# Optimization experiments

Measured on AMD Instinct MI355X. Metric: run time of the kernel, lower is better.

## Reference

```python
import jax, jax.numpy as jnp
import numpy as np

N = 50000      # num nodes
E = 600000     # num edges
D = 128        # num_node_features (in == out)
R = 8          # num_relations


def setup_inputs() -> dict:
    key = jax.random.key(0)
    k = jax.random.split(key, 6)
    x = jax.random.normal(k[0], (N, D), dtype=jnp.float32)
    edge_index = jax.random.randint(k[1], (2, E), 0, N, dtype=jnp.int32)
    edge_type = jax.random.randint(k[2], (E,), 0, R, dtype=jnp.int32)
    scale = 1.0 / np.sqrt(D).astype(np.float32)
    weight = jax.random.normal(k[3], (R, D, D), dtype=jnp.float32) * scale  # per-relation W_r
    root = jax.random.normal(k[4], (D, D), dtype=jnp.float32) * scale       # self-loop weight
    bias = jnp.zeros((D,), dtype=jnp.float32)
    return {"x": x, "edge_index": edge_index, "edge_type": edge_type,
            "weight": weight, "root": root, "bias": bias}


def _rgcn(x, weight, root, bias, edge_index, edge_type):
    # RGCNConv (PyG defaults: aggr='mean' per relation, root weight + bias)
    src, dst = edge_index[0], edge_index[1]
    # combined segment id over (relation, dst) so one segment_sum covers all relations
    seg = edge_type * N + dst                              # [E]
    msgs = x[src]                                          # [E, D] gather
    sums = jax.ops.segment_sum(msgs, seg, num_segments=R * N)                 # [R*N, D]
    cnts = jax.ops.segment_sum(jnp.ones((E, 1), x.dtype), seg, num_segments=R * N)
    mean = sums / jnp.maximum(cnts, 1.0)                   # mean over neighbors, 0 if none
    agg = mean.reshape(R, N, D)
    out = jnp.einsum('rnd,rde->ne', agg, weight) + x @ root + bias
    return out


def reference(x, edge_index, edge_type, weight, root, bias):
    return jax.nn.relu(_rgcn(x, weight, root, bias, edge_index, edge_type))
```

## Files before the change

### kernel.cpp

```cpp
#include <hip/hip_runtime.h>

constexpr int NN = 50000;
constexpr int NE = 600000;
constexpr int D  = 128;
constexpr int NR = 8;
constexpr int KT = (NR + 1) * D;
constexpr int NSEG = NN * NR;

constexpr int SCAN_ELEMS = 1024;
constexpr int NBLK2 = (NSEG + SCAN_ELEMS - 1) / SCAN_ELEMS;

constexpr int BM = 128;
constexpr int GEMM_GRID = (NN + BM - 1) / BM;

typedef unsigned int   u32;
typedef unsigned short u16;
typedef float  f32x4 __attribute__((ext_vector_type(4)));
typedef short  s16x8 __attribute__((ext_vector_type(8)));

__device__ __forceinline__ u16 f2bf(float f) {
    u32 u = __float_as_uint(f);
    u32 r = (u + 0x7fffu + ((u >> 16) & 1u)) >> 16;
    return (u16)r;
}

__device__ __forceinline__ void async_cp16(const void* g, void* l) {
    __builtin_amdgcn_global_load_lds(
        (const __attribute__((address_space(1))) u32*)g,
        (__attribute__((address_space(3))) u32*)l, 16, 0, 0);
}

__global__ __launch_bounds__(256) void prep_all(const float* __restrict__ x,
                                                const float* __restrict__ weight,
                                                const float* __restrict__ root,
                                                const int* __restrict__ dst,
                                                const int* __restrict__ et,
                                                u16* __restrict__ xb,
                                                u16* __restrict__ wt9,
                                                int* __restrict__ cnt2) {
    const int NX4 = NN * D / 4;
    const int NW  = (NR + 1) * D * D;
    int gid = blockIdx.x * 256 + threadIdx.x;
    if (gid < NX4) {
        int i = gid * 4;
        float4 v = *(const float4*)(x + i);
        ushort4 o;
        o.x = f2bf(v.x); o.y = f2bf(v.y); o.z = f2bf(v.z); o.w = f2bf(v.w);
        *(ushort4*)(xb + i) = o;
        return;
    }
    int g = gid - NX4;
    if (g < NW) {
        int p = g >> 14;
        int idx = g & 16383;
        int n = idx >> 7, k = idx & 127;
        float v = (p == 0) ? root[k * D + n]
                           : weight[(size_t)(p - 1) * D * D + k * D + n];
        wt9[(size_t)p * 16384 + idx] = f2bf(v);
        return;
    }
    int e = g - NW;
    if (e < NE) atomicAdd(&cnt2[dst[e] * NR + et[e]], 1);
}

__global__ __launch_bounds__(256) void scan1(const int* __restrict__ cnt,
                                             int* __restrict__ offs,
                                             int* __restrict__ bsums) {
    __shared__ int lds[256];
    int t = threadIdx.x;
    int base = blockIdx.x * SCAN_ELEMS + t * 4;
    int v0 = (base + 0 < NSEG) ? cnt[base + 0] : 0;
    int v1 = (base + 1 < NSEG) ? cnt[base + 1] : 0;
    int v2 = (base + 2 < NSEG) ? cnt[base + 2] : 0;
    int v3 = (base + 3 < NSEG) ? cnt[base + 3] : 0;
    int s = v0 + v1 + v2 + v3;
    lds[t] = s;
    __syncthreads();
    int val = s;
    for (int off = 1; off < 256; off <<= 1) {
        int tmp = (t >= off) ? lds[t - off] : 0;
        __syncthreads();
        val += tmp;
        lds[t] = val;
        __syncthreads();
    }
    int ex = val - s;
    if (base + 0 < NSEG) offs[base + 0] = ex;
    if (base + 1 < NSEG) offs[base + 1] = ex + v0;
    if (base + 2 < NSEG) offs[base + 2] = ex + v0 + v1;
    if (base + 3 < NSEG) offs[base + 3] = ex + v0 + v1 + v2;
    if (t == 255) bsums[blockIdx.x] = val;
}

__global__ __launch_bounds__(512) void scan2(int* __restrict__ bsums) {
    __shared__ int lds[512];
    int t = threadIdx.x;
    int v = (t < NBLK2) ? bsums[t] : 0;
    lds[t] = v;
    __syncthreads();
    int val = v;
    for (int off = 1; off < 512; off <<= 1) {
        int tmp = (t >= off) ? lds[t - off] : 0;
        __syncthreads();
        val += tmp;
        lds[t] = val;
        __syncthreads();
    }
    if (t < NBLK2) bsums[t] = val - v;
}

__global__ __launch_bounds__(256) void scan3(int* __restrict__ offs,
                                             int* __restrict__ cur,
                                             const int* __restrict__ bsums) {
    int i = blockIdx.x * 256 + threadIdx.x;
    if (i < NSEG) {
        int v = offs[i] + bsums[i >> 10];
        offs[i] = v;
        cur[i]  = v;
    }
    if (i == 0) offs[NSEG] = NE;
}

__global__ __launch_bounds__(256) void fill_bins(const int* __restrict__ src,
                                                 const int* __restrict__ dst,
                                                 const int* __restrict__ et,
                                                 int* __restrict__ cur,
                                                 int* __restrict__ ebin) {
    int e = blockIdx.x * 256 + threadIdx.x;
    if (e >= NE) return;
    int r = et[e];
    int idx = atomicAdd(&cur[dst[e] * NR + r], 1);
    ebin[idx] = (r << 16) | src[e];
}

__global__ __launch_bounds__(128) void aggregate_kernel(const u32* __restrict__ xw,
                                                        const int* __restrict__ offs2,
                                                        const int* __restrict__ ebin,
                                                        u32* __restrict__ sw) {
    const int lane = threadIdx.x & 63;
    const int n = blockIdx.x * 2 + (threadIdx.x >> 6);
    if (n >= NN) return;
    const int beg = __builtin_amdgcn_readfirstlane(offs2[n * NR]);
    const int c   = __builtin_amdgcn_readfirstlane(offs2[n * NR + NR]) - beg;

    float a0 = 0.f, a1 = 0.f;
    int r_cur = 0, cnt_cur = 0;

    int q0 = 0, q1 = 0, q2 = 0, q3 = 0, q4 = 0, q5 = 0, q6 = 0, q7 = 0;
    u32 v0 = 0, v1 = 0, v2 = 0, v3 = 0, v4 = 0, v5 = 0, v6 = 0, v7 = 0;

#define REFILL(Q, V, IDX)                                                   \
    if ((IDX) < c) {                                                        \
        Q = __builtin_amdgcn_readfirstlane(ebin[beg + (IDX)]);              \
        V = xw[(size_t)((u32)Q & 0xffffu) * 64 + lane];                     \
    }
#define FLUSH()                                                             \
    {                                                                       \
        float inv_ = 1.0f / (float)(cnt_cur > 0 ? cnt_cur : 1);             \
        u32 lo16_ = f2bf(a0 * inv_);                                        \
        u32 hi16_ = f2bf(a1 * inv_);                                        \
        sw[((size_t)r_cur * NN + n) * 64 + lane] = lo16_ | (hi16_ << 16);   \
        a0 = 0.f; a1 = 0.f; cnt_cur = 0; ++r_cur;                           \
    }
#define CONSUME(Q, V)                                                       \
    {                                                                       \
        int rj_ = (int)((u32)(Q) >> 16);                                    \
        while (r_cur < rj_) FLUSH()                                         \
        a0 += __uint_as_float((V) << 16);                                   \
        a1 += __uint_as_float((V) & 0xffff0000u);                           \
        ++cnt_cur;                                                          \
    }

    REFILL(q0, v0, 0) REFILL(q1, v1, 1) REFILL(q2, v2, 2) REFILL(q3, v3, 3)
    REFILL(q4, v4, 4) REFILL(q5, v5, 5) REFILL(q6, v6, 6) REFILL(q7, v7, 7)

    int e = 0;
    for (; e + 8 <= c; e += 8) {
        CONSUME(q0, v0) REFILL(q0, v0, e + 8)
        CONSUME(q1, v1) REFILL(q1, v1, e + 9)
        CONSUME(q2, v2) REFILL(q2, v2, e + 10)
        CONSUME(q3, v3) REFILL(q3, v3, e + 11)
        CONSUME(q4, v4) REFILL(q4, v4, e + 12)
        CONSUME(q5, v5) REFILL(q5, v5, e + 13)
        CONSUME(q6, v6) REFILL(q6, v6, e + 14)
        CONSUME(q7, v7) REFILL(q7, v7, e + 15)
    }
    if (e + 0 < c) CONSUME(q0, v0)
    if (e + 1 < c) CONSUME(q1, v1)
    if (e + 2 < c) CONSUME(q2, v2)
    if (e + 3 < c) CONSUME(q3, v3)
    if (e + 4 < c) CONSUME(q4, v4)
    if (e + 5 < c) CONSUME(q5, v5)
    if (e + 6 < c) CONSUME(q6, v6)
    if (e + 7 < c) CONSUME(q7, v7)

    while (r_cur < NR) FLUSH()
#undef REFILL
#undef FLUSH
#undef CONSUME
}

__global__ __launch_bounds__(256) void mfma_gemm(const u16* __restrict__ xb,
                                                 const u16* __restrict__ sums,
                                                 const u16* __restrict__ wt9,
                                                 const float* __restrict__ bias,
                                                 float* __restrict__ out) {
    __shared__ __align__(16) u16 Bs[2][128 * 64];

    const int tid  = threadIdx.x;
    const int wave = tid >> 6;
    const int lane = tid & 63;
    const int m0   = blockIdx.x * BM;
    const int fr   = lane & 15;
    const int l4   = lane >> 4;
    const int fk   = l4 * 8;

    int boff[4];
#pragma unroll
    for (int r = 0; r < 4; ++r) {
        int p = r * 256 + tid;
        int g = p ^ ((p >> 3) & 7);
        boff[r] = (g >> 3) * D + (g & 7) * 8;
    }
    int bidx[16];
#pragma unroll
    for (int h = 0; h < 2; ++h)
#pragma unroll
        for (int nt = 0; nt < 8; ++nt) {
            int gl = (nt * 16 + fr) * 8 + h * 4 + l4;
            int pp = gl ^ ((gl >> 3) & 7);
            bidx[h * 8 + nt] = pp * 8;
        }

    int r0 = m0 + wave * 32 + fr;       if (r0 > NN - 1) r0 = NN - 1;
    int r1 = m0 + wave * 32 + 16 + fr;  if (r1 > NN - 1) r1 = NN - 1;
    const size_t aoff0 = (size_t)r0 * D + fk;
    const size_t aoff1 = (size_t)r1 * D + fk;

    auto stage = [&](u16* bufp, const u16* Bp) {
#pragma unroll
        for (int r = 0; r < 4; ++r)
            async_cp16(Bp + boff[r], (char*)bufp + (size_t)(r * 256 + tid) * 16);
    };

    f32x4 acc0[8], acc1[8];
#pragma unroll
    for (int j = 0; j < 8; ++j) {
        acc0[j] = (f32x4){0.f, 0.f, 0.f, 0.f};
        acc1[j] = (f32x4){0.f, 0.f, 0.f, 0.f};
    }

    s16x8 a0c, a1c, a2c, a3c, a0n1, a1n1, a2n1, a3n1, a0n2, a1n2, a2n2, a3n2;

    stage(&Bs[0][0], wt9);
    a0c  = *(const s16x8*)(xb + aoff0);
    a1c  = *(const s16x8*)(xb + aoff0 + 32);
    a2c  = *(const s16x8*)(xb + aoff1);
    a3c  = *(const s16x8*)(xb + aoff1 + 32);
    a0n1 = *(const s16x8*)(xb + aoff0 + 64);
    a1n1 = *(const s16x8*)(xb + aoff0 + 96);
    a2n1 = *(const s16x8*)(xb + aoff1 + 64);
    a3n1 = *(const s16x8*)(xb + aoff1 + 96);
    a0n2 = a0n1; a1n2 = a1n1; a2n2 = a2n1; a3n2 = a3n1;
    __builtin_amdgcn_sched_barrier(0);

    for (int it = 0; it < 17; ++it) {
        const int nx  = it + 1;
        const int npl = nx >> 1;
        const int kof = (nx & 1) * 64;
        u16* nbuf = &Bs[nx & 1][0];
        const u16* cbuf = &Bs[it & 1][0];

        stage(nbuf, wt9 + npl * 16384 + kof);
        if (it + 2 <= 17) {
            const int p2 = (it + 2) >> 1;
            const int k2 = ((it + 2) & 1) * 64;
            const u16* Ap2 = ((p2 == 0) ? xb
                              : sums + (size_t)(p2 - 1) * NN * D) + k2;
            a0n2 = *(const s16x8*)(Ap2 + aoff0);
            a1n2 = *(const s16x8*)(Ap2 + aoff0 + 32);
            a2n2 = *(const s16x8*)(Ap2 + aoff1);
            a3n2 = *(const s16x8*)(Ap2 + aoff1 + 32);
        }
        __builtin_amdgcn_sched_barrier(0);
        if (it < 16) { asm volatile("s_waitcnt vmcnt(12)" ::: "memory"); }
        else         { asm volatile("s_waitcnt vmcnt(8)"  ::: "memory"); }
        __builtin_amdgcn_s_barrier();
        __builtin_amdgcn_sched_barrier(0);
#pragma unroll
        for (int nt = 0; nt < 8; ++nt) {
            s16x8 bf = *(const s16x8*)(cbuf + bidx[nt]);
            acc0[nt] = __builtin_amdgcn_mfma_f32_16x16x32_bf16(a0c, bf, acc0[nt], 0, 0, 0);
            acc1[nt] = __builtin_amdgcn_mfma_f32_16x16x32_bf16(a2c, bf, acc1[nt], 0, 0, 0);
        }
#pragma unroll
        for (int nt = 0; nt < 8; ++nt) {
            s16x8 bf = *(const s16x8*)(cbuf + bidx[8 + nt]);
            acc0[nt] = __builtin_amdgcn_mfma_f32_16x16x32_bf16(a1c, bf, acc0[nt], 0, 0, 0);
            acc1[nt] = __builtin_amdgcn_mfma_f32_16x16x32_bf16(a3c, bf, acc1[nt], 0, 0, 0);
        }
        asm volatile("s_waitcnt lgkmcnt(0)" ::: "memory");
        __builtin_amdgcn_sched_barrier(0);
        __builtin_amdgcn_s_barrier();
        __builtin_amdgcn_sched_barrier(0);
        a0c = a0n1; a1c = a1n1; a2c = a2n1; a3c = a3n1;
        a0n1 = a0n2; a1n1 = a1n2; a2n1 = a2n2; a3n1 = a3n2;
    }
    asm volatile("s_waitcnt vmcnt(0)" ::: "memory");
    __builtin_amdgcn_s_barrier();
    __builtin_amdgcn_sched_barrier(0);
    {
        const u16* cbuf = &Bs[1][0];
#pragma unroll
        for (int nt = 0; nt < 8; ++nt) {
            s16x8 bf = *(const s16x8*)(cbuf + bidx[nt]);
            acc0[nt] = __builtin_amdgcn_mfma_f32_16x16x32_bf16(a0c, bf, acc0[nt], 0, 0, 0);
            acc1[nt] = __builtin_amdgcn_mfma_f32_16x16x32_bf16(a2c, bf, acc1[nt], 0, 0, 0);
        }
#pragma unroll
        for (int nt = 0; nt < 8; ++nt) {
            s16x8 bf = *(const s16x8*)(cbuf + bidx[8 + nt]);
            acc0[nt] = __builtin_amdgcn_mfma_f32_16x16x32_bf16(a1c, bf, acc0[nt], 0, 0, 0);
            acc1[nt] = __builtin_amdgcn_mfma_f32_16x16x32_bf16(a3c, bf, acc1[nt], 0, 0, 0);
        }
    }

    const int cl = lane & 15;
    const int rq = l4 * 4;
#pragma unroll
    for (int nt = 0; nt < 8; ++nt) {
        int col = nt * 16 + cl;
        float bv = bias[col];
#pragma unroll
        for (int reg = 0; reg < 4; ++reg) {
            int n = m0 + wave * 32 + rq + reg;
            if (n < NN) {
                float v = acc0[nt][reg] + bv;
                out[(size_t)n * D + col] = fmaxf(v, 0.0f);
            }
            int n2 = n + 16;
            if (n2 < NN) {
                float v = acc1[nt][reg] + bv;
                out[(size_t)n2 * D + col] = fmaxf(v, 0.0f);
            }
        }
    }
}

extern "C" void kernel_launch(void* const* d_in, const int* in_sizes, int n_in,
                              void* d_out, int out_size, void* d_ws, size_t ws_size,
                              hipStream_t stream) {
    const float* x      = (const float*)d_in[0];
    const int*   ei     = (const int*)d_in[1];
    const int*   et     = (const int*)d_in[2];
    const float* weight = (const float*)d_in[3];
    const float* root   = (const float*)d_in[4];
    const float* bias   = (const float*)d_in[5];
    float* out = (float*)d_out;
    const int* srcv = ei;
    const int* dstv = ei + NE;

    int* cnt2  = (int*)d_ws;
    int* cur2  = cnt2 + NSEG;
    int* offs2 = cur2 + NSEG;
    int* bsums = offs2 + NSEG + 1;
    int* ebin  = bsums + 512;
    size_t fixed_b  = ((char*)(ebin + NE) - (char*)d_ws);
    size_t fixed_al = (fixed_b + 255) & ~(size_t)255;
    u16* xb   = (u16*)((char*)d_ws + fixed_al);
    u16* sums = xb + (size_t)NN * D;
    u16* wt9  = sums + (size_t)NR * NN * D;

    hipMemsetAsync(cnt2, 0, NSEG * sizeof(int), stream);

    const int PREP = NN * D / 4 + (NR + 1) * D * D + NE;
    prep_all<<<(PREP + 255) / 256, 256, 0, stream>>>(x, weight, root, dstv, et,
                                                     xb, wt9, cnt2);

    scan1<<<NBLK2, 256, 0, stream>>>(cnt2, offs2, bsums);
    scan2<<<1, 512, 0, stream>>>(bsums);
    scan3<<<(NSEG + 256) / 256, 256, 0, stream>>>(offs2, cur2, bsums);
    fill_bins<<<(NE + 255) / 256, 256, 0, stream>>>(srcv, dstv, et, cur2, ebin);

    aggregate_kernel<<<(NN + 1) / 2, 128, 0, stream>>>((const u32*)xb, offs2, ebin,
                                                       (u32*)sums);

    mfma_gemm<<<GEMM_GRID, 256, 0, stream>>>(xb, sums, wt9, bias, out);
}
```

Before: 215.8 us.

## Skip storing empty relation segments; GEMM reads a zero page instead

The aggregation kernel no longer writes mean rows for (node, relation) segments that have no edges. The GEMM derives a per-row empty-relation bitmask from the CSR offsets and points the A-fragment loads for those rows at a small zeroed workspace page instead of the sums buffer. This removes both the write and the later read of empty bf16 rows, which are a sizeable share at the average degree here. In exchange each GEMM row does extra offset loads and address selects, and correctness now depends on the zero page staying zeroed.

New measurement: 216.1 us. No clear change (+0.1%).

```diff
diff --git a/kernel.cpp b/kernel.cpp
--- a/kernel.cpp
+++ b/kernel.cpp
@@ -4,7 +4,6 @@
 constexpr int NE = 600000;
 constexpr int D  = 128;
 constexpr int NR = 8;
-constexpr int KT = (NR + 1) * D;
 constexpr int NSEG = NN * NR;
 
 constexpr int SCAN_ELEMS = 1024;
@@ -156,11 +155,14 @@
     }
 #define FLUSH()                                                             \
     {                                                                       \
-        float inv_ = 1.0f / (float)(cnt_cur > 0 ? cnt_cur : 1);             \
-        u32 lo16_ = f2bf(a0 * inv_);                                        \
-        u32 hi16_ = f2bf(a1 * inv_);                                        \
-        sw[((size_t)r_cur * NN + n) * 64 + lane] = lo16_ | (hi16_ << 16);   \
-        a0 = 0.f; a1 = 0.f; cnt_cur = 0; ++r_cur;                           \
+        if (cnt_cur > 0) {                                                  \
+            float inv_ = 1.0f / (float)cnt_cur;                             \
+            u32 lo16_ = f2bf(a0 * inv_);                                    \
+            u32 hi16_ = f2bf(a1 * inv_);                                    \
+            sw[((size_t)r_cur * NN + n) * 64 + lane] = lo16_ | (hi16_ << 16);\
+            a0 = 0.f; a1 = 0.f; cnt_cur = 0;                                \
+        }                                                                   \
+        ++r_cur;                                                            \
     }
 #define CONSUME(Q, V)                                                       \
     {                                                                       \
@@ -204,6 +206,8 @@
                                                  const u16* __restrict__ sums,
                                                  const u16* __restrict__ wt9,
                                                  const float* __restrict__ bias,
+                                                 const int* __restrict__ offs2,
+                                                 const u16* __restrict__ zp,
                                                  float* __restrict__ out) {
     __shared__ __align__(16) u16 Bs[2][128 * 64];
 
@@ -236,6 +240,27 @@
     int r1 = m0 + wave * 32 + 16 + fr;  if (r1 > NN - 1) r1 = NN - 1;
     const size_t aoff0 = (size_t)r0 * D + fk;
     const size_t aoff1 = (size_t)r1 * D + fk;
+
+    u32 emp0, emp1;
+    {
+        const int* q0 = offs2 + r0 * NR;
+        int4 A0 = *(const int4*)q0;
+        int4 B0 = *(const int4*)(q0 + 4);
+        int  C0 = q0[8];
+        emp0 = (u32)(A0.y == A0.x) | ((u32)(A0.z == A0.y) << 1) |
+               ((u32)(A0.w == A0.z) << 2) | ((u32)(B0.x == A0.w) << 3) |
+               ((u32)(B0.y == B0.x) << 4) | ((u32)(B0.z == B0.y) << 5) |
+               ((u32)(B0.w == B0.z) << 6) | ((u32)(C0 == B0.w) << 7);
+        const int* q1 = offs2 + r1 * NR;
+        int4 A1 = *(const int4*)q1;
+        int4 B1 = *(const int4*)(q1 + 4);
+        int  C1 = q1[8];
+        emp1 = (u32)(A1.y == A1.x) | ((u32)(A1.z == A1.y) << 1) |
+               ((u32)(A1.w == A1.z) << 2) | ((u32)(B1.x == A1.w) << 3) |
+               ((u32)(B1.y == B1.x) << 4) | ((u32)(B1.z == B1.y) << 5) |
+               ((u32)(B1.w == B1.z) << 6) | ((u32)(C1 == B1.w) << 7);
+    }
+    __builtin_amdgcn_sched_barrier(0);
 
     auto stage = [&](u16* bufp, const u16* Bp) {
 #pragma unroll
@@ -275,12 +300,14 @@
         if (it + 2 <= 17) {
             const int p2 = (it + 2) >> 1;
             const int k2 = ((it + 2) & 1) * 64;
-            const u16* Ap2 = ((p2 == 0) ? xb
-                              : sums + (size_t)(p2 - 1) * NN * D) + k2;
-            a0n2 = *(const s16x8*)(Ap2 + aoff0);
-            a1n2 = *(const s16x8*)(Ap2 + aoff0 + 32);
-            a2n2 = *(const s16x8*)(Ap2 + aoff1);
-            a3n2 = *(const s16x8*)(Ap2 + aoff1 + 32);
+            const int rel = p2 - 1;
+            const u16* Ap2 = sums + (size_t)rel * NN * D + k2;
+            const u16* b0 = ((emp0 >> rel) & 1) ? zp : Ap2 + aoff0;
+            const u16* b1 = ((emp1 >> rel) & 1) ? zp : Ap2 + aoff1;
+            a0n2 = *(const s16x8*)(b0);
+            a1n2 = *(const s16x8*)(b0 + 32);
+            a2n2 = *(const s16x8*)(b1);
+            a3n2 = *(const s16x8*)(b1 + 32);
         }
         __builtin_amdgcn_sched_barrier(0);
         if (it < 16) { asm volatile("s_waitcnt vmcnt(12)" ::: "memory"); }
@@ -361,7 +388,8 @@
     const int* dstv = ei + NE;
 
     int* cnt2  = (int*)d_ws;
-    int* cur2  = cnt2 + NSEG;
+    int* zpi   = cnt2 + NSEG;
+    int* cur2  = zpi + 128;
     int* offs2 = cur2 + NSEG;
     int* bsums = offs2 + NSEG + 1;
     int* ebin  = bsums + 512;
@@ -371,7 +399,7 @@
     u16* sums = xb + (size_t)NN * D;
     u16* wt9  = sums + (size_t)NR * NN * D;
 
-    hipMemsetAsync(cnt2, 0, NSEG * sizeof(int), stream);
+    (void)hipMemsetAsync(cnt2, 0, (NSEG + 128) * sizeof(int), stream);
 
     const int PREP = NN * D / 4 + (NR + 1) * D * D + NE;
     prep_all<<<(PREP + 255) / 256, 256, 0, stream>>>(x, weight, root, dstv, et,
@@ -385,5 +413,6 @@
     aggregate_kernel<<<(NN + 1) / 2, 128, 0, stream>>>((const u32*)xb, offs2, ebin,
                                                        (u32*)sums);
 
-    mfma_gemm<<<GEMM_GRID, 256, 0, stream>>>(xb, sums, wt9, bias, out);
-}
+    mfma_gemm<<<GEMM_GRID, 256, 0, stream>>>(xb, sums, wt9, bias, offs2,
+                                             (const u16*)zpi, out);
+}
```
